# Performance work log

Hardware: AMD Instinct MI355X
Metric: run time of the kernel (lower is better)

## Reference

```python
import jax, jax.numpy as jnp
import numpy as np

B = 32
H = 56
WD = 56
C = 192
NH = 6
WS = 7   # window size
SS = 3   # shift size
HID = 4 * C
N = WS * WS
NW = (H // WS) * (WD // WS)


def _rel_pos_index():
    coords = np.stack(np.meshgrid(np.arange(WS), np.arange(WS), indexing='ij'))  # [2,ws,ws]
    cf = coords.reshape(2, -1)
    rel = cf[:, :, None] - cf[:, None, :]          # [2,N,N]
    rel = rel.transpose(1, 2, 0)
    rel[..., 0] += WS - 1
    rel[..., 1] += WS - 1
    rel[..., 0] *= 2 * WS - 1
    return rel.sum(-1)                              # [N,N] int


def _attn_mask():
    img = np.zeros((H, WD))
    sl = (slice(0, -WS), slice(-WS, -SS), slice(-SS, None))
    cnt = 0
    for hs in sl:
        for ws in sl:
            img[hs, ws] = cnt
            cnt += 1
    mw = img.reshape(H // WS, WS, WD // WS, WS).transpose(0, 2, 1, 3).reshape(-1, N)  # [nW,N]
    d = mw[:, None, :] - mw[:, :, None]
    return np.where(d != 0, -100.0, 0.0).astype(np.float32)  # [nW,N,N]


_RPI = jnp.asarray(_rel_pos_index())
_MASK = jnp.asarray(_attn_mask())


def setup_inputs() -> dict:
    key = jax.random.key(0)
    ks = jax.random.split(key, 8)
    s = 0.02
    return {
        'x': jax.random.normal(ks[0], (B, H * WD, C), jnp.float32),
        'norm1_g': jnp.ones((C,), jnp.float32),
        'norm1_b': jnp.zeros((C,), jnp.float32),
        'qkv_w': jax.random.normal(ks[1], (C, 3 * C), jnp.float32) * s,
        'qkv_b': jnp.zeros((3 * C,), jnp.float32),
        'rel_bias': jax.random.normal(ks[2], ((2 * WS - 1) ** 2, NH), jnp.float32) * s,
        'proj_w': jax.random.normal(ks[3], (C, C), jnp.float32) * s,
        'proj_b': jnp.zeros((C,), jnp.float32),
        'norm2_g': jnp.ones((C,), jnp.float32),
        'norm2_b': jnp.zeros((C,), jnp.float32),
        'fc1_w': jax.random.normal(ks[4], (C, HID), jnp.float32) * s,
        'fc1_b': jnp.zeros((HID,), jnp.float32),
        'fc2_w': jax.random.normal(ks[5], (HID, C), jnp.float32) * s,
        'fc2_b': jnp.zeros((C,), jnp.float32),
    }


def _ln(x, g, b, eps=1e-5):
    m = jnp.mean(x, axis=-1, keepdims=True)
    v = jnp.mean(jnp.square(x - m), axis=-1, keepdims=True)
    return (x - m) / jnp.sqrt(v + eps) * g + b


def reference(x, norm1_g, norm1_b, qkv_w, qkv_b, rel_bias, proj_w, proj_b,
              norm2_g, norm2_b, fc1_w, fc1_b, fc2_w, fc2_b):
    hd = C // NH
    shortcut = x
    xn = _ln(x, norm1_g, norm1_b).reshape(B, H, WD, C)
    xs = jnp.roll(xn, (-SS, -SS), axis=(1, 2))                     # cyclic shift
    # window partition -> [B*nW, N, C]
    xw = xs.reshape(B, H // WS, WS, WD // WS, WS, C)
    xw = xw.transpose(0, 1, 3, 2, 4, 5).reshape(-1, N, C)
    # windowed attention
    qkv = (xw @ qkv_w + qkv_b).reshape(-1, N, 3, NH, hd).transpose(2, 0, 3, 1, 4)
    q, k, v = qkv[0], qkv[1], qkv[2]                               # [B*nW, NH, N, hd]
    attn = jnp.einsum('whnd,whmd->whnm', q * (hd ** -0.5), k)      # [B*nW, NH, N, N]
    bias = rel_bias[_RPI.reshape(-1)].reshape(N, N, NH).transpose(2, 0, 1)
    attn = attn + bias[None]
    attn = attn.reshape(B, NW, NH, N, N) + _MASK[None, :, None]
    attn = jax.nn.softmax(attn.reshape(-1, NH, N, N), axis=-1)
    out = jnp.einsum('whnm,whmd->whnd', attn, v)
    out = out.transpose(0, 2, 1, 3).reshape(-1, N, C)
    out = out @ proj_w + proj_b
    # window reverse + un-shift
    out = out.reshape(B, H // WS, WD // WS, WS, WS, C)
    out = out.transpose(0, 1, 3, 2, 4, 5).reshape(B, H, WD, C)
    out = jnp.roll(out, (SS, SS), axis=(1, 2)).reshape(B, H * WD, C)
    x = shortcut + out
    # MLP (exact GELU, matching torch nn.GELU default)
    xm = _ln(x, norm2_g, norm2_b)
    h = jax.nn.gelu(xm @ fc1_w + fc1_b, approximate=False)
    return x + (h @ fc2_w + fc2_b)
```

## Files before the change

kernel.cpp:

```cpp
#include <hip/hip_runtime.h>
#include <math.h>


constexpr long T = 100352;

typedef __attribute__((ext_vector_type(8))) short short8;
typedef __attribute__((ext_vector_type(4))) float f32x4;

__device__ __forceinline__ short bf16(float f) {
    union { float f; unsigned u; } v; v.f = f;
    return (short)((v.u + 0x7fff + ((v.u >> 16) & 1)) >> 16);
}

__device__ __forceinline__ void gll16(const void* g, void* l) {
    __builtin_amdgcn_global_load_lds(
        (const __attribute__((address_space(1))) void*)g,
        (__attribute__((address_space(3))) void*)l, 16, 0, 0);
}

__global__ __launch_bounds__(256)
void prep_k(const float* __restrict__ qkv_w, const float* __restrict__ proj_w,
            const float* __restrict__ fc1_w, const float* __restrict__ fc2_w,
            const float* __restrict__ relb, const float* __restrict__ x,
            short* __restrict__ qkvP, short* __restrict__ projP,
            short* __restrict__ fc1P, short* __restrict__ fc2P,
            float* __restrict__ bm, float* __restrict__ mean,
            float* __restrict__ rstd)
{
    const int bid = blockIdx.x;
    const int tid = threadIdx.x;
    if (bid < 432) {
        const int idx = bid * 256 + tid;
        const int k = idx / 576, n = idx - k * 576;
        const int flat = (((n >> 4) * 6 + (k >> 5)) * 64 +
                          (((k >> 3) & 3) << 4) + (n & 15)) * 8 + (k & 7);
        qkvP[flat] = bf16(qkv_w[idx]);
    } else if (bid < 576) {
        const int idx = (bid - 432) * 256 + tid;
        const int k = idx / 192, n = idx - k * 192;
        const int flat = ((((k >> 5) * 12 + (n >> 4)) * 64) +
                          (((k >> 3) & 3) << 4) + (n & 15)) * 8 + (k & 7);
        projP[flat] = bf16(proj_w[idx]);
    } else if (bid < 1152) {
        const int idx = (bid - 576) * 256 + tid;
        const int k = idx / 768, n = idx - k * 768;
        const int flat = (((n >> 4) * 6 + (k >> 5)) * 64 +
                          (((k >> 3) & 3) << 4) + (n & 15)) * 8 + (k & 7);
        fc1P[flat] = bf16(fc1_w[idx]);
    } else if (bid < 1728) {
        const int idx = (bid - 1152) * 256 + tid;
        const int k = idx / 192, n = idx - k * 192;
        const int t = k >> 6, ks = (k >> 5) & 1, nt = n >> 4;
        const int flat = ((((t * 12 + nt) << 1) + ks) * 64 +
                          (((k >> 3) & 3) << 4) + (n & 15)) * 8 + (k & 7);
        fc2P[flat] = bf16(fc2_w[idx]);
    } else if (bid < 1954) {
        const int idx = (bid - 1728) * 256 + tid;
        if (idx >= 6 * 4 * 2401) return;
        const int e = idx % 2401, rest = idx / 2401;
        const int tw = rest & 1, th = (rest >> 1) & 1, head = rest >> 2;
        const int i = e / 49, j = e - i * 49;
        const int yi = i / 7, xi = i - yi * 7, yj = j / 7, xj = j - yj * 7;
        const float v = relb[((yi - yj + 6) * 13 + (xi - xj + 6)) * 6 + head];
        const int hi = th ? 49 + yi : yi, hj = th ? 49 + yj : yj;
        const int wa = tw ? 49 + xi : xi, wb = tw ? 49 + xj : xj;
        const int Li = (hi < 49 ? 0 : (hi < 53 ? 1 : 2)) * 3 + (wa < 49 ? 0 : (wa < 53 ? 1 : 2));
        const int Lj = (hj < 49 ? 0 : (hj < 53 ? 1 : 2)) * 3 + (wb < 49 ? 0 : (wb < 53 ? 1 : 2));
        bm[idx] = (Li != Lj) ? v - 100.0f : v;
    } else {
        const int wave = tid >> 6;
        const int lane = tid & 63;
        const long tok = (long)(bid - 1954) * 4 + wave;
        const float* p = x + tok * 192;
        const float a = p[lane], b = p[lane + 64], c = p[lane + 128];
        float s = a + b + c;
        float q = a * a + b * b + c * c;
        #pragma unroll
        for (int off = 32; off > 0; off >>= 1) {
            s += __shfl_xor(s, off);
            q += __shfl_xor(q, off);
        }
        if (lane == 0) {
            const float m = s * (1.0f / 192.0f);
            const float v = q * (1.0f / 192.0f) - m * m;
            mean[tok] = m;
            rstd[tok] = 1.0f / sqrtf(v + 1e-5f);
        }
    }
}

__global__ __launch_bounds__(256, 3)
void winattn_k(const float* __restrict__ x, const float* __restrict__ n1g,
               const float* __restrict__ n1b, const short* __restrict__ qkvP,
               const float* __restrict__ qkv_b, const float* __restrict__ bm,
               const float* __restrict__ mean, const float* __restrict__ rstd,
               float* __restrict__ outp)
{
    __shared__ __align__(16) short Kb[2][2048];
    __shared__ __align__(16) short Vb[2][2048];
    __shared__ __align__(16) short Pf[4][1024];
    const int bw  = blockIdx.x;
    const int tid = threadIdx.x;
    const int b = bw >> 6, wi = bw & 63, wh = wi >> 3, ww = wi & 7;
    const int wave = tid >> 6, lane = tid & 63;
    const int col = lane & 15, rbase = (lane >> 4) << 2;
    const float scale = 0.17677669529663687f;

    const int am = lane & 15;
    const int arow = (wave << 4) + am;
    const int kof = (lane >> 4) << 3;
    short8 afr[6];
    long tokA = 0; float mA = 0.f, rsA = 1.f;
    const bool avalid = arow < 49;
    if (avalid) {
        const int yi = arow / 7, xi = arow - yi * 7;
        int h = wh * 7 + yi + 3; if (h >= 56) h -= 56;
        int w = ww * 7 + xi + 3; if (w >= 56) w -= 56;
        tokA = (long)b * 3136 + h * 56 + w;
        mA = mean[tokA]; rsA = rstd[tokA];
    }
    #pragma unroll
    for (int ks = 0; ks < 6; ++ks) {
        short8 a = {};
        if (avalid) {
            const int k0 = (ks << 5) + kof;
            const float4 v0 = *(const float4*)(x + tokA * 192 + k0);
            const float4 v1 = *(const float4*)(x + tokA * 192 + k0 + 4);
            const float4 g0 = *(const float4*)(n1g + k0);
            const float4 g1 = *(const float4*)(n1g + k0 + 4);
            const float4 e0 = *(const float4*)(n1b + k0);
            const float4 e1 = *(const float4*)(n1b + k0 + 4);
            a[0] = bf16((v0.x - mA) * rsA * g0.x + e0.x);
            a[1] = bf16((v0.y - mA) * rsA * g0.y + e0.y);
            a[2] = bf16((v0.z - mA) * rsA * g0.z + e0.z);
            a[3] = bf16((v0.w - mA) * rsA * g0.w + e0.w);
            a[4] = bf16((v1.x - mA) * rsA * g1.x + e1.x);
            a[5] = bf16((v1.y - mA) * rsA * g1.y + e1.y);
            a[6] = bf16((v1.z - mA) * rsA * g1.z + e1.z);
            a[7] = bf16((v1.w - mA) * rsA * g1.w + e1.w);
        }
        afr[ks] = a;
    }

    short8 qfrag[6];
    #pragma unroll
    for (int nt = 0; nt < 12; ++nt) {
        f32x4 acc = {};
        #pragma unroll
        for (int ks = 0; ks < 6; ++ks) {
            const short8 bfr = *(const short8*)(qkvP + ((nt * 6 + ks) * 64 + lane) * 8);
            acc = __builtin_amdgcn_mfma_f32_16x16x32_bf16(afr[ks], bfr, acc, 0, 0, 0);
        }
        const int hh = nt >> 1, d = ((nt & 1) << 4) + col;
        const float bias = qkv_b[hh * 32 + d];
        #pragma unroll
        for (int r = 0; r < 4; ++r) {
            const int m = rbase + r;
            Pf[wave][((m + (((d >> 3) & 3) << 4)) << 3) + (d & 7)] =
                bf16((acc[r] + bias) * scale);
        }
        if (nt & 1) qfrag[hh] = *(const short8*)&Pf[wave][lane << 3];
    }

    long tok_r[4]; bool iv[4]; int i49[4];
    #pragma unroll
    for (int r = 0; r < 4; ++r) {
        const int i = (wave << 4) + rbase + r;
        iv[r] = i < 49;
        i49[r] = iv[r] ? i * 49 : 0;
        if (iv[r]) {
            const int yi = i / 7, xi = i - yi * 7;
            int h = wh * 7 + yi + 3; if (h >= 56) h -= 56;
            int w = ww * 7 + xi + 3; if (w >= 56) w -= 56;
            tok_r[r] = (long)b * 3136 + h * 56 + w;
        } else tok_r[r] = 0;
    }

    f32x4 oa[12] = {};

    #pragma unroll
    for (int h = 0; h < 6; ++h) {
        const int bs = h & 1;
        #pragma unroll
        for (int half = 0; half < 2; ++half) {
            const int d = (half << 4) + col;
            f32x4 acck = {};
            #pragma unroll
            for (int ks = 0; ks < 6; ++ks) {
                const short8 bfr = *(const short8*)(qkvP +
                    (((12 + 2 * h + half) * 6 + ks) * 64 + lane) * 8);
                acck = __builtin_amdgcn_mfma_f32_16x16x32_bf16(afr[ks], bfr, acck, 0, 0, 0);
            }
            const float biask = qkv_b[192 + h * 32 + d];
            #pragma unroll
            for (int r = 0; r < 4; ++r) {
                const int m = rbase + r;
                Kb[bs][(((wave << 6) + m + (((d >> 3) & 3) << 4)) << 3) + (d & 7)] =
                    bf16(acck[r] + biask);
            }
            f32x4 accv = {};
            #pragma unroll
            for (int ks = 0; ks < 6; ++ks) {
                const short8 bfr = *(const short8*)(qkvP +
                    (((24 + 2 * h + half) * 6 + ks) * 64 + lane) * 8);
                accv = __builtin_amdgcn_mfma_f32_16x16x32_bf16(afr[ks], bfr, accv, 0, 0, 0);
            }
            const float biasv = qkv_b[384 + h * 32 + d];
            #pragma unroll
            for (int r = 0; r < 4; ++r) {
                const int m = rbase + r;
                const int flat = ((((half << 1) + (wave >> 1)) << 6) + col +
                                  ((((wave << 1) + (m >> 3)) & 3) << 4)) * 8 + (m & 7);
                Vb[bs][flat] = bf16(accv[r] + biasv);
            }
        }
        __syncthreads();

        const float* bmp = bm + (((h << 1) + (wh == 7)) * 2 + (ww == 7)) * 2401;
        f32x4 sa[4];
        #pragma unroll
        for (int jt = 0; jt < 4; ++jt) {
            f32x4 z = {};
            const short8 kfr = *(const short8*)&Kb[bs][((jt << 6) + lane) << 3];
            sa[jt] = __builtin_amdgcn_mfma_f32_16x16x32_bf16(qfrag[h], kfr, z, 0, 0, 0);
        }
        float p[4][4];
        #pragma unroll
        for (int jt = 0; jt < 4; ++jt) {
            const int j = (jt << 4) + col;
            #pragma unroll
            for (int r = 0; r < 4; ++r)
                p[jt][r] = (j < 49) ? sa[jt][r] + bmp[i49[r] + j] : -1e30f;
        }
        #pragma unroll
        for (int r = 0; r < 4; ++r) {
            float mx = fmaxf(fmaxf(p[0][r], p[1][r]), fmaxf(p[2][r], p[3][r]));
            mx = fmaxf(mx, __shfl_xor(mx, 1));
            mx = fmaxf(mx, __shfl_xor(mx, 2));
            mx = fmaxf(mx, __shfl_xor(mx, 4));
            mx = fmaxf(mx, __shfl_xor(mx, 8));
            float sum = 0.f;
            #pragma unroll
            for (int jt = 0; jt < 4; ++jt) {
                const float e = (((jt << 4) + col) < 49) ? __expf(p[jt][r] - mx) : 0.f;
                p[jt][r] = e; sum += e;
            }
            sum += __shfl_xor(sum, 1);
            sum += __shfl_xor(sum, 2);
            sum += __shfl_xor(sum, 4);
            sum += __shfl_xor(sum, 8);
            const float inv = 1.0f / sum;
            #pragma unroll
            for (int jt = 0; jt < 4; ++jt) p[jt][r] *= inv;
        }
        #pragma unroll
        for (int jt = 0; jt < 4; ++jt) {
            #pragma unroll
            for (int r = 0; r < 4; ++r) {
                const int m = rbase + r;
                const int flat = (((jt >> 1) << 6) + m +
                                  ((((jt & 1) << 1) + (col >> 3)) << 4)) * 8 + (col & 7);
                Pf[wave][flat] = bf16(p[jt][r]);
            }
        }
        const short8 p0 = *(const short8*)&Pf[wave][lane << 3];
        const short8 p1 = *(const short8*)&Pf[wave][(64 + lane) << 3];
        #pragma unroll
        for (int dt = 0; dt < 2; ++dt) {
            const short8 v0 = *(const short8*)&Vb[bs][(((dt << 1) << 6) + lane) << 3];
            const short8 v1 = *(const short8*)&Vb[bs][((((dt << 1) + 1) << 6) + lane) << 3];
            oa[h * 2 + dt] = __builtin_amdgcn_mfma_f32_16x16x32_bf16(p0, v0, oa[h * 2 + dt], 0, 0, 0);
            oa[h * 2 + dt] = __builtin_amdgcn_mfma_f32_16x16x32_bf16(p1, v1, oa[h * 2 + dt], 0, 0, 0);
        }
    }

    #pragma unroll
    for (int r = 0; r < 4; ++r) {
        if (!iv[r]) continue;
        float* op = outp + tok_r[r] * 192;
        #pragma unroll
        for (int hh = 0; hh < 6; ++hh) {
            op[hh * 32 + col]      = oa[hh * 2 + 0][r];
            op[hh * 32 + 16 + col] = oa[hh * 2 + 1][r];
        }
    }
}

__global__ __launch_bounds__(256, 3)
void projmlp_k(const float* attnb, const short* __restrict__ projP,
               const float* __restrict__ pb, const float* __restrict__ x,
               const float* __restrict__ n2g, const float* __restrict__ n2b,
               const short* __restrict__ fc1P, const float* __restrict__ b1,
               const short* __restrict__ fc2P, const float* __restrict__ b2,
               float* outp)
{
    __shared__ __align__(16) short S1[12288];
    __shared__ __align__(16) short S2[12288];
    __shared__ __align__(16) short Hs[2048];
    const int tid = threadIdx.x;
    const int wave = tid >> 6, lane = tid & 63;
    const int col = lane & 15, rbase = (lane >> 4) << 2;
    const int kof = (lane >> 4) << 3;
    const long m0 = (long)blockIdx.x * 64;

    const long arow = m0 + (wave << 4) + col;
    const float* ap = attnb + arow * 192;
    short8 afr[6];
    #pragma unroll
    for (int ks = 0; ks < 6; ++ks) {
        const int k0 = (ks << 5) + kof;
        const float4 v0 = *(const float4*)(ap + k0);
        const float4 v1 = *(const float4*)(ap + k0 + 4);
        short8 a;
        a[0] = bf16(v0.x); a[1] = bf16(v0.y); a[2] = bf16(v0.z); a[3] = bf16(v0.w);
        a[4] = bf16(v1.x); a[5] = bf16(v1.y); a[6] = bf16(v1.z); a[7] = bf16(v1.w);
        afr[ks] = a;
    }
    f32x4 x1a[12] = {};
    #pragma unroll
    for (int ks = 0; ks < 6; ++ks) {
        #pragma unroll
        for (int nt = 0; nt < 12; ++nt) {
            const short8 bfr = *(const short8*)(projP + ks * 6144 + (nt << 9) + (lane << 3));
            x1a[nt] = __builtin_amdgcn_mfma_f32_16x16x32_bf16(afr[ks], bfr, x1a[nt], 0, 0, 0);
        }
    }
    const long orow = m0 + (wave << 4) + rbase;
    #pragma unroll
    for (int nt = 0; nt < 12; ++nt) {
        const int n = (nt << 4) + col;
        const float bias = pb[n];
        #pragma unroll
        for (int r = 0; r < 4; ++r)
            x1a[nt][r] += bias + x[(orow + r) * 192 + n];
    }
    float s0 = 0.f, s1_ = 0.f, s2_ = 0.f, s3 = 0.f;
    float q0 = 0.f, q1 = 0.f, q2 = 0.f, q3 = 0.f;
    #pragma unroll
    for (int nt = 0; nt < 12; ++nt) {
        s0 += x1a[nt][0]; q0 += x1a[nt][0] * x1a[nt][0];
        s1_ += x1a[nt][1]; q1 += x1a[nt][1] * x1a[nt][1];
        s2_ += x1a[nt][2]; q2 += x1a[nt][2] * x1a[nt][2];
        s3 += x1a[nt][3]; q3 += x1a[nt][3] * x1a[nt][3];
    }
    #pragma unroll
    for (int off = 8; off > 0; off >>= 1) {
        s0 += __shfl_xor(s0, off); q0 += __shfl_xor(q0, off);
        s1_ += __shfl_xor(s1_, off); q1 += __shfl_xor(q1, off);
        s2_ += __shfl_xor(s2_, off); q2 += __shfl_xor(q2, off);
        s3 += __shfl_xor(s3, off); q3 += __shfl_xor(q3, off);
    }
    float mr[4], rr[4];
    mr[0] = s0 * (1.0f / 192.0f); rr[0] = rsqrtf(q0 * (1.0f / 192.0f) - mr[0] * mr[0] + 1e-5f);
    mr[1] = s1_ * (1.0f / 192.0f); rr[1] = rsqrtf(q1 * (1.0f / 192.0f) - mr[1] * mr[1] + 1e-5f);
    mr[2] = s2_ * (1.0f / 192.0f); rr[2] = rsqrtf(q2 * (1.0f / 192.0f) - mr[2] * mr[2] + 1e-5f);
    mr[3] = s3 * (1.0f / 192.0f); rr[3] = rsqrtf(q3 * (1.0f / 192.0f) - mr[3] * mr[3] + 1e-5f);

    short* Xw = S1 + wave * 3072;
    #pragma unroll
    for (int nt = 0; nt < 12; ++nt) {
        const int k = (nt << 4) + col;
        const float g = n2g[k], bb = n2b[k];
        #pragma unroll
        for (int r = 0; r < 4; ++r) {
            const int row16 = rbase + r;
            const int flat = (((k >> 5) << 6) + (((k >> 3) & 3) << 4) + row16) * 8 + (k & 7);
            Xw[flat] = bf16((x1a[nt][r] - mr[r]) * rr[r] * g + bb);
        }
    }
    short8 afrX[6];
    #pragma unroll
    for (int ks = 0; ks < 6; ++ks)
        afrX[ks] = *(const short8*)(Xw + (((ks << 6) + lane) << 3));

    f32x4 accO[12];
    #pragma unroll
    for (int nt = 0; nt < 12; ++nt) {
        const float bias = b2[(nt << 4) + col];
        #pragma unroll
        for (int r = 0; r < 4; ++r)
            accO[nt][r] = x1a[nt][r] + bias;
    }

    short* Hw = Hs + wave * 512;
    for (int t = 0; t < 12; ++t) {
        __syncthreads();
        {
            const short* f1 = fc1P + t * 12288;
            const short* f2 = fc2P + t * 12288;
            #pragma unroll
            for (int i = 0; i < 6; ++i) {
                const int slot = (i << 8) + (wave << 6);
                gll16(f1 + ((slot + lane) << 3), S1 + (slot << 3));
                gll16(f2 + ((slot + lane) << 3), S2 + (slot << 3));
            }
        }
        __syncthreads();
        f32x4 accH[4] = {};
        #pragma unroll
        for (int ks = 0; ks < 6; ++ks) {
            #pragma unroll
            for (int nt = 0; nt < 4; ++nt) {
                const short8 bfr = *(const short8*)&S1[((nt * 6 + ks) << 9) + (lane << 3)];
                accH[nt] = __builtin_amdgcn_mfma_f32_16x16x32_bf16(afrX[ks], bfr, accH[nt], 0, 0, 0);
            }
        }
        #pragma unroll
        for (int hf = 0; hf < 2; ++hf) {
            #pragma unroll
            for (int ntl = 0; ntl < 2; ++ntl) {
                const int nt = (hf << 1) + ntl;
                const int kh = (nt << 4) + col;
                const float bias = b1[(t << 6) + kh];
                #pragma unroll
                for (int r = 0; r < 4; ++r) {
                    const int m = rbase + r;
                    float val = accH[nt][r] + bias;
                    val = 0.5f * val * (1.0f + erff(val * 0.7071067811865476f));
                    const int flat = ((((kh >> 3) & 3) << 4) + m) * 8 + (kh & 7);
                    Hw[flat] = bf16(val);
                }
            }
            const short8 a = *(const short8*)(Hw + (lane << 3));
            #pragma unroll
            for (int nt2 = 0; nt2 < 12; ++nt2) {
                const short8 bfr = *(const short8*)&S2[(((nt2 << 1) + hf) << 9) + (lane << 3)];
                accO[nt2] = __builtin_amdgcn_mfma_f32_16x16x32_bf16(a, bfr, accO[nt2], 0, 0, 0);
            }
        }
    }

    #pragma unroll
    for (int nt = 0; nt < 12; ++nt) {
        const int n = (nt << 4) + col;
        #pragma unroll
        for (int r = 0; r < 4; ++r)
            outp[(orow + r) * 192 + n] = accO[nt][r];
    }
}

extern "C" void kernel_launch(void* const* d_in, const int* in_sizes, int n_in,
                              void* d_out, int out_size, void* d_ws, size_t ws_size,
                              hipStream_t stream)
{
    const float* x      = (const float*)d_in[0];
    const float* n1g    = (const float*)d_in[1];
    const float* n1b    = (const float*)d_in[2];
    const float* qkv_w  = (const float*)d_in[3];
    const float* qkv_b  = (const float*)d_in[4];
    const float* relb   = (const float*)d_in[5];
    const float* proj_w = (const float*)d_in[6];
    const float* proj_b = (const float*)d_in[7];
    const float* n2g    = (const float*)d_in[8];
    const float* n2b    = (const float*)d_in[9];
    const float* fc1_w  = (const float*)d_in[10];
    const float* fc1_b  = (const float*)d_in[11];
    const float* fc2_w  = (const float*)d_in[12];
    const float* fc2_b  = (const float*)d_in[13];
    float* out = (float*)d_out;
    char*  ws  = (char*)d_ws;

    float* mb    = (float*)(ws);
    float* rb    = (float*)(ws +   401408L);
    short* qkvP  = (short*)(ws +   802816L);
    short* projP = (short*)(ws +  1024000L);
    short* fc1P  = (short*)(ws +  1097728L);
    short* fc2P  = (short*)(ws +  1392640L);
    float* bmT   = (float*)(ws +  1687552L);

    prep_k<<<1954 + T / 4, 256, 0, stream>>>(qkv_w, proj_w, fc1_w, fc2_w,
                                             relb, x, qkvP, projP, fc1P,
                                             fc2P, bmT, mb, rb);
    winattn_k<<<2048, 256, 0, stream>>>(x, n1g, n1b, qkvP, qkv_b,
                                        bmT, mb, rb, out);
    projmlp_k<<<T / 64, 256, 0, stream>>>(out, projP, proj_b, x, n2g, n2b,
                                          fc1P, fc1_b, fc2P, fc2_b, out);
}
```

Baseline: 450.7 us.

## Double-buffer MLP weight tiles in LDS to overlap loads with MFMA

The fused proj+MLP kernel now streams fc1/fc2 weight chunks through two half-size LDS buffers. The next chunk is prefetched with global_load_lds while MFMAs run on the current one, replacing the old load-all-then-compute pattern. The fc2 packing layout is reordered so each half-chunk is contiguous. LDS use shrinks, which could raise occupancy, but each iteration now has four barriers, and it depends on the async load finishing before each barrier.

```diff
diff --git a/kernel.cpp b/kernel.cpp
--- a/kernel.cpp
+++ b/kernel.cpp
@@ -51,7 +51,7 @@
         const int idx = (bid - 1152) * 256 + tid;
         const int k = idx / 192, n = idx - k * 192;
         const int t = k >> 6, ks = (k >> 5) & 1, nt = n >> 4;
-        const int flat = ((((t * 12 + nt) << 1) + ks) * 64 +
+        const int flat = (((t * 2 + ks) * 12 + nt) * 64 +
                           (((k >> 3) & 3) << 4) + (n & 15)) * 8 + (k & 7);
         fc2P[flat] = bf16(fc2_w[idx]);
     } else if (bid < 1954) {
@@ -294,8 +294,7 @@
                const short* __restrict__ fc2P, const float* __restrict__ b2,
                float* outp)
 {
-    __shared__ __align__(16) short S1[12288];
-    __shared__ __align__(16) short S2[12288];
+    __shared__ __align__(16) short SB[2][6144];
     __shared__ __align__(16) short Hs[2048];
     const int tid = threadIdx.x;
     const int wave = tid >> 6, lane = tid & 63;
@@ -356,7 +355,7 @@
     mr[2] = s2_ * (1.0f / 192.0f); rr[2] = rsqrtf(q2 * (1.0f / 192.0f) - mr[2] * mr[2] + 1e-5f);
     mr[3] = s3 * (1.0f / 192.0f); rr[3] = rsqrtf(q3 * (1.0f / 192.0f) - mr[3] * mr[3] + 1e-5f);
 
-    short* Xw = S1 + wave * 3072;
+    short* Xw = (short*)SB + wave * 3072;
     #pragma unroll
     for (int nt = 0; nt < 12; ++nt) {
         const int k = (nt << 4) + col;
@@ -381,53 +380,89 @@
         for (int r = 0; r < 4; ++r)
             accO[nt][r] = x1a[nt][r] + bias;
     }
-
+    __syncthreads();
+
+    auto STAGE = [&](short* dst, const short* src) {
+        #pragma unroll
+        for (int i = 0; i < 3; ++i) {
+            const int slot = (i << 8) + (wave << 6);
+            gll16(src + ((slot + lane) << 3), dst + (slot << 3));
+        }
+    };
     short* Hw = Hs + wave * 512;
+    STAGE(SB[0], fc1P);
+    __syncthreads();
+    int cur = 0;
     for (int t = 0; t < 12; ++t) {
-        __syncthreads();
+        const short* f1 = fc1P + t * 12288;
+        const short* f2 = fc2P + t * 12288;
+        f32x4 accH[4] = {};
+        STAGE(SB[cur ^ 1], f1 + 6144);
+        #pragma unroll
+        for (int ks = 0; ks < 6; ++ks) {
+            #pragma unroll
+            for (int ntl = 0; ntl < 2; ++ntl) {
+                const short8 bfr = *(const short8*)&SB[cur][((ntl * 6 + ks) << 9) + (lane << 3)];
+                accH[ntl] = __builtin_amdgcn_mfma_f32_16x16x32_bf16(afrX[ks], bfr, accH[ntl], 0, 0, 0);
+            }
+        }
+        __syncthreads(); cur ^= 1;
+        STAGE(SB[cur ^ 1], f2);
+        #pragma unroll
+        for (int ks = 0; ks < 6; ++ks) {
+            #pragma unroll
+            for (int ntl = 0; ntl < 2; ++ntl) {
+                const short8 bfr = *(const short8*)&SB[cur][((ntl * 6 + ks) << 9) + (lane << 3)];
+                accH[2 + ntl] = __builtin_amdgcn_mfma_f32_16x16x32_bf16(afrX[ks], bfr, accH[2 + ntl], 0, 0, 0);
+            }
+        }
+        __syncthreads(); cur ^= 1;
+        STAGE(SB[cur ^ 1], f2 + 6144);
+        #pragma unroll
+        for (int nt = 0; nt < 2; ++nt) {
+            const int kh = (nt << 4) + col;
+            const float bias = b1[(t << 6) + kh];
+            #pragma unroll
+            for (int r = 0; r < 4; ++r) {
+                const int m = rbase + r;
+                float val = accH[nt][r] + bias;
+                val = 0.5f * val * (1.0f + erff(val * 0.7071067811865476f));
+                const int flat = ((((kh >> 3) & 3) << 4) + m) * 8 + (kh & 7);
+                Hw[flat] = bf16(val);
+            }
+        }
         {
-            const short* f1 = fc1P + t * 12288;
-            const short* f2 = fc2P + t * 12288;
-            #pragma unroll
-            for (int i = 0; i < 6; ++i) {
-                const int slot = (i << 8) + (wave << 6);
-                gll16(f1 + ((slot + lane) << 3), S1 + (slot << 3));
-                gll16(f2 + ((slot + lane) << 3), S2 + (slot << 3));
-            }
-        }
-        __syncthreads();
-        f32x4 accH[4] = {};
-        #pragma unroll
-        for (int ks = 0; ks < 6; ++ks) {
-            #pragma unroll
-            for (int nt = 0; nt < 4; ++nt) {
-                const short8 bfr = *(const short8*)&S1[((nt * 6 + ks) << 9) + (lane << 3)];
-                accH[nt] = __builtin_amdgcn_mfma_f32_16x16x32_bf16(afrX[ks], bfr, accH[nt], 0, 0, 0);
-            }
-        }
-        #pragma unroll
-        for (int hf = 0; hf < 2; ++hf) {
-            #pragma unroll
-            for (int ntl = 0; ntl < 2; ++ntl) {
-                const int nt = (hf << 1) + ntl;
-                const int kh = (nt << 4) + col;
-                const float bias = b1[(t << 6) + kh];
-                #pragma unroll
-                for (int r = 0; r < 4; ++r) {
-                    const int m = rbase + r;
-                    float val = accH[nt][r] + bias;
-                    val = 0.5f * val * (1.0f + erff(val * 0.7071067811865476f));
-                    const int flat = ((((kh >> 3) & 3) << 4) + m) * 8 + (kh & 7);
-                    Hw[flat] = bf16(val);
-                }
-            }
             const short8 a = *(const short8*)(Hw + (lane << 3));
             #pragma unroll
             for (int nt2 = 0; nt2 < 12; ++nt2) {
-                const short8 bfr = *(const short8*)&S2[(((nt2 << 1) + hf) << 9) + (lane << 3)];
+                const short8 bfr = *(const short8*)&SB[cur][(nt2 << 9) + (lane << 3)];
                 accO[nt2] = __builtin_amdgcn_mfma_f32_16x16x32_bf16(a, bfr, accO[nt2], 0, 0, 0);
             }
         }
+        __syncthreads(); cur ^= 1;
+        if (t < 11) STAGE(SB[cur ^ 1], f1 + 12288);
+        #pragma unroll
+        for (int nt = 2; nt < 4; ++nt) {
+            const int kh = (nt << 4) + col;
+            const float bias = b1[(t << 6) + kh];
+            #pragma unroll
+            for (int r = 0; r < 4; ++r) {
+                const int m = rbase + r;
+                float val = accH[nt][r] + bias;
+                val = 0.5f * val * (1.0f + erff(val * 0.7071067811865476f));
+                const int flat = ((((kh >> 3) & 3) << 4) + m) * 8 + (kh & 7);
+                Hw[flat] = bf16(val);
+            }
+        }
+        {
+            const short8 a = *(const short8*)(Hw + (lane << 3));
+            #pragma unroll
+            for (int nt2 = 0; nt2 < 12; ++nt2) {
+                const short8 bfr = *(const short8*)&SB[cur][(nt2 << 9) + (lane << 3)];
+                accO[nt2] = __builtin_amdgcn_mfma_f32_16x16x32_bf16(a, bfr, accO[nt2], 0, 0, 0);
+            }
+        }
+        __syncthreads(); cur ^= 1;
     }
 
     #pragma unroll
```

After: 463.3 us. +2.8%, slower.

## Fuse window attention with projection and MLP into one kernel per window

Applied to the files above, without the earlier changes.

Merges the attention kernel and the proj+MLP kernel so each 64-row window block keeps attention outputs in registers, converts them to bf16 A fragments through LDS, and runs proj, LN2, fc1, GELU and fc2 before writing the final output. This removes the fp32 round trip of the attention result through global memory and one kernel launch. Shared memory is unioned across phases, and the fc2 packing layout is reordered to match. The trade-off is that only 49 of 64 rows per block are valid, which wastes MFMA work on padding, and the larger LDS footprint and register pressure may reduce occupancy.

```diff
diff --git a/kernel.cpp b/kernel.cpp
--- a/kernel.cpp
+++ b/kernel.cpp
@@ -51,7 +51,7 @@
         const int idx = (bid - 1152) * 256 + tid;
         const int k = idx / 192, n = idx - k * 192;
         const int t = k >> 6, ks = (k >> 5) & 1, nt = n >> 4;
-        const int flat = ((((t * 12 + nt) << 1) + ks) * 64 +
+        const int flat = (((t * 2 + ks) * 12 + nt) * 64 +
                           (((k >> 3) & 3) << 4) + (n & 15)) * 8 + (k & 7);
         fc2P[flat] = bf16(fc2_w[idx]);
     } else if (bid < 1954) {
@@ -90,15 +90,24 @@
 }
 
 __global__ __launch_bounds__(256, 3)
-void winattn_k(const float* __restrict__ x, const float* __restrict__ n1g,
+void winfull_k(const float* __restrict__ x, const float* __restrict__ n1g,
                const float* __restrict__ n1b, const short* __restrict__ qkvP,
                const float* __restrict__ qkv_b, const float* __restrict__ bm,
                const float* __restrict__ mean, const float* __restrict__ rstd,
+               const short* __restrict__ projP, const float* __restrict__ pb,
+               const float* __restrict__ n2g, const float* __restrict__ n2b,
+               const short* __restrict__ fc1P, const float* __restrict__ b1,
+               const short* __restrict__ fc2P, const float* __restrict__ b2,
                float* __restrict__ outp)
 {
-    __shared__ __align__(16) short Kb[2][2048];
-    __shared__ __align__(16) short Vb[2][2048];
-    __shared__ __align__(16) short Pf[4][1024];
+    __shared__ __align__(16) char LU[53248];
+    short (*Kb)[2048] = (short (*)[2048])(LU);
+    short (*Vb)[2048] = (short (*)[2048])(LU + 8192);
+    short (*Pf)[1024] = (short (*)[1024])(LU + 16384);
+    short* S1  = (short*)LU;
+    short* S2  = (short*)(LU + 24576);
+    short* HsB = (short*)(LU + 49152);
+
     const int bw  = blockIdx.x;
     const int tid = threadIdx.x;
     const int b = bw >> 6, wi = bw & 63, wh = wi >> 3, ww = wi & 7;
@@ -274,66 +283,40 @@
         }
     }
 
-    #pragma unroll
-    for (int r = 0; r < 4; ++r) {
-        if (!iv[r]) continue;
-        float* op = outp + tok_r[r] * 192;
-        #pragma unroll
-        for (int hh = 0; hh < 6; ++hh) {
-            op[hh * 32 + col]      = oa[hh * 2 + 0][r];
-            op[hh * 32 + 16 + col] = oa[hh * 2 + 1][r];
-        }
-    }
-}
-
-__global__ __launch_bounds__(256, 3)
-void projmlp_k(const float* attnb, const short* __restrict__ projP,
-               const float* __restrict__ pb, const float* __restrict__ x,
-               const float* __restrict__ n2g, const float* __restrict__ n2b,
-               const short* __restrict__ fc1P, const float* __restrict__ b1,
-               const short* __restrict__ fc2P, const float* __restrict__ b2,
-               float* outp)
-{
-    __shared__ __align__(16) short S1[12288];
-    __shared__ __align__(16) short S2[12288];
-    __shared__ __align__(16) short Hs[2048];
-    const int tid = threadIdx.x;
-    const int wave = tid >> 6, lane = tid & 63;
-    const int col = lane & 15, rbase = (lane >> 4) << 2;
-    const int kof = (lane >> 4) << 3;
-    const long m0 = (long)blockIdx.x * 64;
-
-    const long arow = m0 + (wave << 4) + col;
-    const float* ap = attnb + arow * 192;
-    short8 afr[6];
-    #pragma unroll
-    for (int ks = 0; ks < 6; ++ks) {
-        const int k0 = (ks << 5) + kof;
-        const float4 v0 = *(const float4*)(ap + k0);
-        const float4 v1 = *(const float4*)(ap + k0 + 4);
-        short8 a;
-        a[0] = bf16(v0.x); a[1] = bf16(v0.y); a[2] = bf16(v0.z); a[3] = bf16(v0.w);
-        a[4] = bf16(v1.x); a[5] = bf16(v1.y); a[6] = bf16(v1.z); a[7] = bf16(v1.w);
-        afr[ks] = a;
-    }
+    short8 afrA[6];
+    #pragma unroll
+    for (int g = 0; g < 6; ++g) {
+        #pragma unroll
+        for (int dt = 0; dt < 2; ++dt) {
+            const int d = (dt << 4) + col;
+            #pragma unroll
+            for (int r = 0; r < 4; ++r) {
+                const int m = rbase + r;
+                Pf[wave][((m + (((d >> 3) & 3) << 4)) << 3) + (d & 7)] =
+                    bf16(oa[g * 2 + dt][r]);
+            }
+        }
+        afrA[g] = *(const short8*)&Pf[wave][lane << 3];
+    }
+
     f32x4 x1a[12] = {};
     #pragma unroll
     for (int ks = 0; ks < 6; ++ks) {
         #pragma unroll
         for (int nt = 0; nt < 12; ++nt) {
             const short8 bfr = *(const short8*)(projP + ks * 6144 + (nt << 9) + (lane << 3));
-            x1a[nt] = __builtin_amdgcn_mfma_f32_16x16x32_bf16(afr[ks], bfr, x1a[nt], 0, 0, 0);
-        }
-    }
-    const long orow = m0 + (wave << 4) + rbase;
+            x1a[nt] = __builtin_amdgcn_mfma_f32_16x16x32_bf16(afrA[ks], bfr, x1a[nt], 0, 0, 0);
+        }
+    }
     #pragma unroll
     for (int nt = 0; nt < 12; ++nt) {
         const int n = (nt << 4) + col;
         const float bias = pb[n];
         #pragma unroll
         for (int r = 0; r < 4; ++r)
-            x1a[nt][r] += bias + x[(orow + r) * 192 + n];
-    }
+            x1a[nt][r] += bias + x[tok_r[r] * 192 + n];
+    }
+
     float s0 = 0.f, s1_ = 0.f, s2_ = 0.f, s3 = 0.f;
     float q0 = 0.f, q1 = 0.f, q2 = 0.f, q3 = 0.f;
     #pragma unroll
@@ -356,7 +339,9 @@
     mr[2] = s2_ * (1.0f / 192.0f); rr[2] = rsqrtf(q2 * (1.0f / 192.0f) - mr[2] * mr[2] + 1e-5f);
     mr[3] = s3 * (1.0f / 192.0f); rr[3] = rsqrtf(q3 * (1.0f / 192.0f) - mr[3] * mr[3] + 1e-5f);
 
-    short* Xw = S1 + wave * 3072;
+    __syncthreads();
+
+    short* Xw = (short*)LU + wave * 3072;
     #pragma unroll
     for (int nt = 0; nt < 12; ++nt) {
         const int k = (nt << 4) + col;
@@ -382,7 +367,7 @@
             accO[nt][r] = x1a[nt][r] + bias;
     }
 
-    short* Hw = Hs + wave * 512;
+    short* Hw = HsB + wave * 512;
     for (int t = 0; t < 12; ++t) {
         __syncthreads();
         {
@@ -424,7 +409,7 @@
             const short8 a = *(const short8*)(Hw + (lane << 3));
             #pragma unroll
             for (int nt2 = 0; nt2 < 12; ++nt2) {
-                const short8 bfr = *(const short8*)&S2[(((nt2 << 1) + hf) << 9) + (lane << 3)];
+                const short8 bfr = *(const short8*)&S2[((hf * 12 + nt2) << 9) + (lane << 3)];
                 accO[nt2] = __builtin_amdgcn_mfma_f32_16x16x32_bf16(a, bfr, accO[nt2], 0, 0, 0);
             }
         }
@@ -435,7 +420,8 @@
         const int n = (nt << 4) + col;
         #pragma unroll
         for (int r = 0; r < 4; ++r)
-            outp[(orow + r) * 192 + n] = accO[nt][r];
+            if (iv[r])
+                outp[tok_r[r] * 192 + n] = accO[nt][r];
     }
 }
 
@@ -471,8 +457,7 @@
     prep_k<<<1954 + T / 4, 256, 0, stream>>>(qkv_w, proj_w, fc1_w, fc2_w,
                                              relb, x, qkvP, projP, fc1P,
                                              fc2P, bmT, mb, rb);
-    winattn_k<<<2048, 256, 0, stream>>>(x, n1g, n1b, qkvP, qkv_b,
-                                        bmT, mb, rb, out);
-    projmlp_k<<<T / 64, 256, 0, stream>>>(out, projP, proj_b, x, n2g, n2b,
-                                          fc1P, fc1_b, fc2P, fc2_b, out);
+    winfull_k<<<2048, 256, 0, stream>>>(x, n1g, n1b, qkvP, qkv_b, bmT,
+                                        mb, rb, projP, proj_b, n2g, n2b,
+                                        fc1P, fc1_b, fc2P, fc2_b, out);
 }
```

Measured after the change: 447.5 us. About the same (-0.7%).
